# Optimization experiments

Measured on AMD Instinct MI355X. Metric: run time of the kernel, lower is better.

Reference implementation:

```python
import jax, jax.numpy as jnp
import numpy as np
import math

B, NG, LS, E = 2, 8, 512, 1024
NH = 16
HD = E // NH
EPS = 1e-6


def rms_norm(x, w):
    xf = x.astype(jnp.float32)
    n = xf * jax.lax.rsqrt(jnp.mean(xf * xf, axis=-1, keepdims=True) + EPS)
    return n.astype(x.dtype) * w


def rotate(x):
    # pairs (a,b) -> (-b, a), matching view(...,-1,2).flip(-1); x[...,0]*=-1
    x2 = x.reshape(*x.shape[:-1], HD // 2, 2)
    out = jnp.stack([-x2[..., 1], x2[..., 0]], axis=-1)
    return out.reshape(x.shape)


def setup_inputs() -> dict:
    key = jax.random.key(0)
    k1, k2, k3 = jax.random.split(key, 3)
    x = jax.random.normal(k1, (B, NG, LS, E), dtype=jnp.float32)
    W_qkv = jax.random.normal(k2, (E, 3 * E), dtype=jnp.float32) * (1.0 / math.sqrt(E))
    ln_w = jnp.ones((E,), dtype=jnp.float32)
    W_proj = jax.random.normal(k3, (E, E), dtype=jnp.float32) * (1.0 / math.sqrt(E))
    return {"x": x, "W_qkv": W_qkv, "ln_w": ln_w, "W_proj": W_proj}


def reference(x, W_qkv, ln_w, W_proj):
    b, ng, ls, _ = x.shape
    qkv = jnp.einsum('bgsc,ce->bgse', x, W_qkv)  # fused QKV projection
    q, k, v = jnp.split(qkv, 3, axis=-1)
    # QK RMSNorm over full embedding dim (before head split)
    q = rms_norm(q, ln_w)
    k = rms_norm(k, ln_w)
    # [B, ng, nh, ls, hd]
    q = q.reshape(b, ng, ls, NH, HD).swapaxes(2, 3)
    k = k.reshape(b, ng, ls, NH, HD).swapaxes(2, 3)
    v = v.reshape(b, ng, ls, NH, HD).swapaxes(2, 3)
    # RoPE (repo's variant: angles duplicated across halves, adjacent-pair rotate)
    pos = 10000.0 ** ((-2.0 * jnp.arange(0, HD, 2, dtype=jnp.float32) - 1.0) / HD)
    token_seq = jnp.arange(ls, dtype=jnp.float32)[:, None] * pos[None, :]  # [ls, hd/2]
    rot = jnp.concatenate([token_seq, token_seq], axis=-1)  # [ls, hd]
    cos, sin = jnp.cos(rot), jnp.sin(rot)
    q = q * cos + rotate(q) * sin
    k = k * cos + rotate(k) * sin
    # causal attention, scale = 1/sqrt(head_dim) (muP=False)
    scale = 1.0 / math.sqrt(HD)
    scores = jnp.einsum('bgnqd,bgnkd->bgnqk', q, k) * scale
    causal = jnp.tril(jnp.ones((ls, ls), dtype=bool))
    scores = jnp.where(causal, scores, jnp.finfo(scores.dtype).min)
    att = jax.nn.softmax(scores, axis=-1)
    y = jnp.einsum('bgnqk,bgnkd->bgnqd', att, v)
    y = y.swapaxes(2, 3).reshape(b, ng, ls, E)
    y = jnp.einsum('bgse,ef->bgsf', y, W_proj)
    return y
```

## Files before the change

kernel.cpp:

```cpp
#include <hip/hip_runtime.h>

typedef unsigned short u16;
typedef unsigned int   u32;
typedef __attribute__((ext_vector_type(8))) short bf16x8;
typedef __attribute__((ext_vector_type(4))) float f32x4;

#define MFMA16(a,b,c) __builtin_amdgcn_mfma_f32_16x16x32_bf16((a),(b),(c),0,0,0)
#define GLD16(gp, lp) __builtin_amdgcn_global_load_lds((const __attribute__((address_space(1))) u32*)(gp), (__attribute__((address_space(3))) u32*)(lp), 16, 0, 0)

#define B_   2
#define NG_  8
#define LS_  512
#define E_   1024
#define NH_  16
#define HD_  64
#define NTOK 8192

__device__ __forceinline__ u16 f2bu(float f){
  u32 u = __builtin_bit_cast(u32, f);
  u32 r = u + 0x7FFFu + ((u >> 16) & 1u);
  return (u16)(r >> 16);
}
__device__ __forceinline__ float b2f(u16 h){
  u32 u = ((u32)h) << 16;
  return __builtin_bit_cast(float, u);
}
__device__ __forceinline__ u32 pk2(float lo, float hi){
  u32 r; asm("v_cvt_pk_bf16_f32 %0, %1, %2" : "=v"(r) : "v"(lo), "v"(hi)); return r;
}

__global__ __launch_bounds__(256) void k_conv_x(const float* __restrict__ x, u16* __restrict__ xb){
  int i = blockIdx.x * 256 + threadIdx.x;
  float4 v = ((const float4*)x)[i];
  ((ushort4*)xb)[i] = make_ushort4(f2bu(v.x), f2bu(v.y), f2bu(v.z), f2bu(v.w));
}

__global__ __launch_bounds__(256) void k_transpose(const float* __restrict__ W, u16* __restrict__ WT,
                                                   int Kd, int Nd){
  __shared__ float tile[32][33];
  int tx = threadIdx.x & 31, ty = threadIdx.x >> 5;
  int c0 = blockIdx.x * 32, r0 = blockIdx.y * 32;
  #pragma unroll
  for (int i = 0; i < 4; i++)
    tile[ty + i*8][tx] = W[(size_t)(r0 + ty + i*8) * Nd + c0 + tx];
  __syncthreads();
  #pragma unroll
  for (int i = 0; i < 4; i++)
    WT[(size_t)(c0 + ty + i*8) * Kd + r0 + tx] = f2bu(tile[tx][ty + i*8]);
}

__global__ __launch_bounds__(256) void k_rope_table(float* __restrict__ ct, float* __restrict__ st){
  int i = blockIdx.x * 256 + threadIdx.x;
  int s = i >> 6, d = i & 63, j = d & 31;
  float freq = powf(10000.f, -(4.f * (float)j + 1.f) / 64.f);
  float th = (float)s * freq;
  ct[i] = cosf(th);
  st[i] = sinf(th);
}

template <typename OutT>
__global__ __launch_bounds__(256, 2) void k_gemm_bt(const u16* __restrict__ A, const u16* __restrict__ Bt,
                                                    OutT* __restrict__ C, int M, int N, int K){
  int nbn = N >> 7;
  int cpx = gridDim.x >> 3;
  int bid = (blockIdx.x & 7) * cpx + (blockIdx.x >> 3);
  int tm = bid / nbn, tn = bid % nbn;
  int tid = threadIdx.x;
  int w = tid >> 6, l = tid & 63;
  int lr = l & 15, lg = l >> 4;
  int wm = (w >> 1) * 64, wn = (w & 1) * 64;

  __shared__ u16 smem[2][2][128 * 64];

  const u16* Ab = A  + (size_t)(tm * 128) * K;
  const u16* Bb = Bt + (size_t)(tn * 128) * K;
  int NT = K >> 6;

  int srow0 = tid >> 3, ssl = tid & 7;
  auto stage = [&](int t, int s){
    int k0 = t << 6;
    #pragma unroll
    for (int q = 0; q < 4; q++){
      int row = q * 32 + srow0;
      int sc  = (ssl ^ (row & 7)) << 3;
      GLD16(Ab + (size_t)row * K + k0 + sc, &smem[s][0][q * 2048 + tid * 8]);
    }
    #pragma unroll
    for (int q = 0; q < 4; q++){
      int row = q * 32 + srow0;
      int sc  = (ssl ^ (row & 7)) << 3;
      GLD16(Bb + (size_t)row * K + k0 + sc, &smem[s][1][q * 2048 + tid * 8]);
    }
  };

  f32x4 acc[4][4] = {};

  stage(0, 0);
  stage(1, 1);
  asm volatile("s_waitcnt vmcnt(8)" ::: "memory");
  asm volatile("s_barrier" ::: "memory");

  for (int t = 0; t < NT; t++){
    int s = t & 1;
    const u16* As = smem[s][0];
    const u16* Bs = smem[s][1];
    bf16x8 bfr[4][2], afr[2][2];
    #pragma unroll
    for (int j = 0; j < 4; j++){
      int rb = wn + j * 16 + lr;
      #pragma unroll
      for (int kk = 0; kk < 2; kk++)
        bfr[j][kk] = *(const bf16x8*)&Bs[rb * 64 + ((kk * 32 + lg * 8) ^ ((rb & 7) << 3))];
    }
    #pragma unroll
    for (int i = 0; i < 2; i++){
      int ra = wm + i * 16 + lr;
      #pragma unroll
      for (int kk = 0; kk < 2; kk++)
        afr[i][kk] = *(const bf16x8*)&As[ra * 64 + ((kk * 32 + lg * 8) ^ ((ra & 7) << 3))];
    }
    __builtin_amdgcn_s_setprio(1);
    #pragma unroll
    for (int i = 0; i < 2; i++)
      #pragma unroll
      for (int j = 0; j < 4; j++){
        acc[i][j] = MFMA16(afr[i][0], bfr[j][0], acc[i][j]);
        acc[i][j] = MFMA16(afr[i][1], bfr[j][1], acc[i][j]);
      }
    __builtin_amdgcn_s_setprio(0);
    asm volatile("s_barrier" ::: "memory");
    #pragma unroll
    for (int i = 0; i < 2; i++){
      int ra = wm + (i + 2) * 16 + lr;
      #pragma unroll
      for (int kk = 0; kk < 2; kk++)
        afr[i][kk] = *(const bf16x8*)&As[ra * 64 + ((kk * 32 + lg * 8) ^ ((ra & 7) << 3))];
    }
    __builtin_amdgcn_s_setprio(1);
    #pragma unroll
    for (int i = 0; i < 2; i++)
      #pragma unroll
      for (int j = 0; j < 4; j++){
        acc[i + 2][j] = MFMA16(afr[i][0], bfr[j][0], acc[i + 2][j]);
        acc[i + 2][j] = MFMA16(afr[i][1], bfr[j][1], acc[i + 2][j]);
      }
    __builtin_amdgcn_s_setprio(0);
    asm volatile("s_barrier" ::: "memory");
    if (t + 2 < NT){
      stage(t + 2, s);
      asm volatile("s_waitcnt vmcnt(8)" ::: "memory");
      asm volatile("s_barrier" ::: "memory");
    } else if (t + 2 == NT){
      asm volatile("s_waitcnt vmcnt(0)" ::: "memory");
      asm volatile("s_barrier" ::: "memory");
    }
  }

  #pragma unroll
  for (int i = 0; i < 4; i++)
    #pragma unroll
    for (int j = 0; j < 4; j++)
      #pragma unroll
      for (int r = 0; r < 4; r++){
        int row = tm * 128 + wm + i * 16 + lg * 4 + r;
        int col = tn * 128 + wn + j * 16 + lr;
        float v = acc[i][j][r];
        if constexpr (sizeof(OutT) == 2) C[(size_t)row * N + col] = f2bu(v);
        else                             C[(size_t)row * N + col] = v;
      }
}

__global__ __launch_bounds__(256) void k_norm_rope(const u16* __restrict__ qkv, const float* __restrict__ lnw,
                                                   const float* __restrict__ ct, const float* __restrict__ st,
                                                   u16* __restrict__ qh, u16* __restrict__ kh, u16* __restrict__ vh){
  int tok = blockIdx.x;
  int t = threadIdx.x;
  int s = tok & (LS_ - 1);
  int bg = tok >> 9;
  const u16* row = qkv + (size_t)tok * 3072;
  int e0 = t * 4;

  ushort4 q4 = *(const ushort4*)&row[e0];
  ushort4 k4 = *(const ushort4*)&row[1024 + e0];
  ushort4 v4 = *(const ushort4*)&row[2048 + e0];
  float qf[4] = {b2f(q4.x), b2f(q4.y), b2f(q4.z), b2f(q4.w)};
  float kf[4] = {b2f(k4.x), b2f(k4.y), b2f(k4.z), b2f(k4.w)};

  float qss = 0.f, kss = 0.f;
  #pragma unroll
  for (int j = 0; j < 4; j++){ qss += qf[j]*qf[j]; kss += kf[j]*kf[j]; }
  #pragma unroll
  for (int o = 32; o; o >>= 1){ qss += __shfl_down(qss, o); kss += __shfl_down(kss, o); }
  __shared__ float redq[4], redk[4];
  if ((t & 63) == 0){ redq[t >> 6] = qss; redk[t >> 6] = kss; }
  __syncthreads();
  float qsum = redq[0] + redq[1] + redq[2] + redq[3];
  float ksum = redk[0] + redk[1] + redk[2] + redk[3];
  float qr = rsqrtf(qsum * (1.f / 1024.f) + 1e-6f);
  float kr = rsqrtf(ksum * (1.f / 1024.f) + 1e-6f);

  float qn[4], kn[4];
  #pragma unroll
  for (int j = 0; j < 4; j++){
    float wv = lnw[e0 + j];
    qn[j] = qf[j] * qr * wv;
    kn[j] = kf[j] * kr * wv;
  }
  int d0 = e0 & 63, h = e0 >> 6;
  const float* cr = ct + s * 64 + d0;
  const float* sr = st + s * 64 + d0;
  float qo[4], ko[4];
  #pragma unroll
  for (int p = 0; p < 4; p += 2){
    float c0 = cr[p], s0 = sr[p], c1 = cr[p+1], s1 = sr[p+1];
    qo[p]   = qn[p]   * c0 - qn[p+1] * s0;
    qo[p+1] = qn[p+1] * c1 + qn[p]   * s1;
    ko[p]   = kn[p]   * c0 - kn[p+1] * s0;
    ko[p+1] = kn[p+1] * c1 + kn[p]   * s1;
  }
  size_t oidx = (((size_t)bg * NH_ + h) * LS_ + s) * HD_ + d0;
  *(ushort4*)&qh[oidx] = make_ushort4(f2bu(qo[0]*0.125f), f2bu(qo[1]*0.125f), f2bu(qo[2]*0.125f), f2bu(qo[3]*0.125f));
  *(ushort4*)&kh[oidx] = make_ushort4(f2bu(ko[0]), f2bu(ko[1]), f2bu(ko[2]), f2bu(ko[3]));
  *(ushort4*)&vh[oidx] = v4;
}

__global__ __launch_bounds__(256) void k_vt(const u16* __restrict__ vh, u16* __restrict__ vt){
  int head = blockIdx.x >> 3, sb = blockIdx.x & 7;
  int s0 = sb * 64;
  __shared__ u16 t[64 * 72];
  const u16* src = vh + (size_t)head * LS_ * HD_ + (size_t)s0 * HD_;
  u16* dst = vt + (size_t)head * HD_ * LS_;
  #pragma unroll
  for (int p = 0; p < 2; p++){
    int idx = p * 256 + threadIdx.x;
    int r = idx >> 3, c8 = (idx & 7) * 8;
    *(bf16x8*)&t[r * 72 + c8] = *(const bf16x8*)&src[r * HD_ + c8];
  }
  __syncthreads();
  #pragma unroll
  for (int p = 0; p < 2; p++){
    int idx = p * 256 + threadIdx.x;
    int d = idx >> 3, s8 = (idx & 7) * 8;
    u16 tmp[8];
    #pragma unroll
    for (int j = 0; j < 8; j++) tmp[j] = t[(s8 + j) * 72 + d];
    *(bf16x8*)&dst[(size_t)d * LS_ + s0 + s8] = *(bf16x8*)tmp;
  }
}

__global__ __launch_bounds__(64) void k_attn(const u16* __restrict__ qh, const u16* __restrict__ kh,
                                             const u16* __restrict__ vt, u16* __restrict__ ytok){
  int bid = blockIdx.x;
  int head = bid & 255;
  int j = 15 - (bid >> 8);
  int l = threadIdx.x & 63;
  int lr = l & 15, lg = l >> 4;
  int q0 = j * 32;
  int ntw = (j >> 1) + 1;

  const u16* Qp = qh + (size_t)head * LS_ * HD_;
  const u16* Kp = kh + (size_t)head * LS_ * HD_;
  const u16* Vp = vt + (size_t)head * HD_ * LS_;
  int bg = head >> 4, h = head & 15;
  u16* Yb = ytok + (size_t)bg * LS_ * E_ + h * HD_;

  bf16x8 aq[2][2];
  #pragma unroll
  for (int mi = 0; mi < 2; mi++)
    #pragma unroll
    for (int kk = 0; kk < 2; kk++)
      aq[mi][kk] = *(const bf16x8*)&Qp[(q0 + mi*16 + lr) * 64 + kk * 32 + lg * 8];

  __shared__ u16 Pw[32 * 72];

  f32x4 o[2][4] = {};
  float mrun[2] = {-1e30f, -1e30f}, lrun[2] = {0.f, 0.f};

  bf16x8 kr[4][2];
  auto loadK = [&](int kv0){
    #pragma unroll
    for (int nk = 0; nk < 4; nk++){
      kr[nk][0] = *(const bf16x8*)&Kp[(kv0 + nk*16 + lr) * 64 + lg * 8];
      kr[nk][1] = *(const bf16x8*)&Kp[(kv0 + nk*16 + lr) * 64 + 32 + lg * 8];
    }
  };
  loadK(0);

  for (int tkv = 0; tkv < ntw; tkv++){
    int kv0 = tkv * 64;
    f32x4 sa[2][4] = {};
    __builtin_amdgcn_s_setprio(1);
    #pragma unroll
    for (int nk = 0; nk < 4; nk++)
      #pragma unroll
      for (int mi = 0; mi < 2; mi++){
        sa[mi][nk] = MFMA16(kr[nk][0], aq[mi][0], sa[mi][nk]);
        sa[mi][nk] = MFMA16(kr[nk][1], aq[mi][1], sa[mi][nk]);
      }
    __builtin_amdgcn_s_setprio(0);
    if (tkv + 1 < ntw) loadK(kv0 + 64);
    bf16x8 vr[4][2];
    #pragma unroll
    for (int nd = 0; nd < 4; nd++){
      vr[nd][0] = *(const bf16x8*)&Vp[(nd*16 + lr) * 512 + kv0 + lg * 8];
      vr[nd][1] = *(const bf16x8*)&Vp[(nd*16 + lr) * 512 + kv0 + 32 + lg * 8];
    }
    if (kv0 + 63 > q0){
      #pragma unroll
      for (int mi = 0; mi < 2; mi++){
        int qg = q0 + mi*16 + lr;
        #pragma unroll
        for (int nk = 0; nk < 4; nk++)
          #pragma unroll
          for (int r = 0; r < 4; r++){
            int kg = kv0 + nk*16 + lg*4 + r;
            if (kg > qg) sa[mi][nk][r] = -1e30f;
          }
      }
    }
    float pmax[2];
    #pragma unroll
    for (int mi = 0; mi < 2; mi++){
      float pm = sa[mi][0][0];
      #pragma unroll
      for (int nk = 0; nk < 4; nk++)
        #pragma unroll
        for (int r = 0; r < 4; r++) pm = fmaxf(pm, sa[mi][nk][r]);
      pm = fmaxf(pm, __shfl_xor(pm, 16));
      pm = fmaxf(pm, __shfl_xor(pm, 32));
      pmax[mi] = pm;
    }
    float dm = fmaxf(pmax[0] - mrun[0], pmax[1] - mrun[1]);
    if (!__all(dm <= 8.f)){
      float alpha[2];
      #pragma unroll
      for (int mi = 0; mi < 2; mi++){
        float mnew = fmaxf(mrun[mi], pmax[mi]);
        alpha[mi] = __expf(mrun[mi] - mnew);
        mrun[mi] = mnew;
        lrun[mi] *= alpha[mi];
      }
      #pragma unroll
      for (int r = 0; r < 4; r++){
        float a0 = __shfl(alpha[0], lg * 4 + r);
        float a1 = __shfl(alpha[1], lg * 4 + r);
        #pragma unroll
        for (int nd = 0; nd < 4; nd++){ o[0][nd][r] *= a0; o[1][nd][r] *= a1; }
      }
    }
    #pragma unroll
    for (int mi = 0; mi < 2; mi++){
      float psum = 0.f;
      #pragma unroll
      for (int nk = 0; nk < 4; nk++)
        #pragma unroll
        for (int r = 0; r < 4; r++){
          float pv = __expf(sa[mi][nk][r] - mrun[mi]);
          sa[mi][nk][r] = pv;
          psum += pv;
        }
      psum += __shfl_xor(psum, 16);
      psum += __shfl_xor(psum, 32);
      lrun[mi] += psum;
    }
    #pragma unroll
    for (int mi = 0; mi < 2; mi++)
      #pragma unroll
      for (int nk = 0; nk < 4; nk++){
        *(u32*)&Pw[(mi*16 + lr) * 72 + nk * 16 + lg * 4]     = pk2(sa[mi][nk][0], sa[mi][nk][1]);
        *(u32*)&Pw[(mi*16 + lr) * 72 + nk * 16 + lg * 4 + 2] = pk2(sa[mi][nk][2], sa[mi][nk][3]);
      }
    bf16x8 pa[2][2];
    #pragma unroll
    for (int mi = 0; mi < 2; mi++){
      pa[mi][0] = *(const bf16x8*)&Pw[(mi*16 + lr) * 72 + lg * 8];
      pa[mi][1] = *(const bf16x8*)&Pw[(mi*16 + lr) * 72 + 32 + lg * 8];
    }
    __builtin_amdgcn_s_setprio(1);
    #pragma unroll
    for (int nd = 0; nd < 4; nd++)
      #pragma unroll
      for (int mi = 0; mi < 2; mi++){
        o[mi][nd] = MFMA16(pa[mi][0], vr[nd][0], o[mi][nd]);
        o[mi][nd] = MFMA16(pa[mi][1], vr[nd][1], o[mi][nd]);
      }
    __builtin_amdgcn_s_setprio(0);
  }

  #pragma unroll
  for (int mi = 0; mi < 2; mi++){
    float linv = 1.f / lrun[mi];
    #pragma unroll
    for (int r = 0; r < 4; r++){
      float ir = __shfl(linv, lg * 4 + r);
      int qg = q0 + mi*16 + lg * 4 + r;
      #pragma unroll
      for (int nd = 0; nd < 4; nd++)
        Yb[(size_t)qg * E_ + nd * 16 + lr] = f2bu(o[mi][nd][r] * ir);
    }
  }
}

extern "C" void kernel_launch(void* const* d_in, const int* in_sizes, int n_in,
                              void* d_out, int out_size, void* d_ws, size_t ws_size,
                              hipStream_t stream){
  const float* x     = (const float*)d_in[0];
  const float* Wqkv  = (const float*)d_in[1];
  const float* lnw   = (const float*)d_in[2];
  const float* Wproj = (const float*)d_in[3];
  float* out = (float*)d_out;

  u16* p = (u16*)d_ws;
  u16* xb     = p; p += (size_t)NTOK * E_;
  u16* wqkvT  = p; p += (size_t)3 * E_ * E_;
  u16* wprojT = p; p += (size_t)E_ * E_;
  u16* qkv    = p; p += (size_t)NTOK * 3 * E_;
  u16* qhp    = p; p += (size_t)NTOK * E_;
  u16* khp    = p; p += (size_t)NTOK * E_;
  u16* vhp    = p; p += (size_t)NTOK * E_;
  float* ct = (float*)p;
  float* st = ct + LS_ * HD_;
  u16* vtp = qkv;

  k_conv_x<<<8192, 256, 0, stream>>>(x, xb);
  k_transpose<<<dim3(96, 32), 256, 0, stream>>>(Wqkv, wqkvT, 1024, 3072);
  k_transpose<<<dim3(32, 32), 256, 0, stream>>>(Wproj, wprojT, 1024, 1024);
  k_rope_table<<<128, 256, 0, stream>>>(ct, st);
  k_gemm_bt<u16><<<64 * 24, 256, 0, stream>>>(xb, wqkvT, qkv, NTOK, 3 * E_, E_);
  k_norm_rope<<<NTOK, 256, 0, stream>>>(qkv, lnw, ct, st, qhp, khp, vhp);
  k_vt<<<2048, 256, 0, stream>>>(vhp, vtp);
  k_attn<<<4096, 64, 0, stream>>>(qhp, khp, vtp, xb);
  k_gemm_bt<float><<<64 * 8, 256, 0, stream>>>(xb, wprojT, out, NTOK, E_, E_);
}
```

Baseline: 166.6 us.

## Enlarge GEMM tiles to 128x256 with 8 waves and triple-buffered B

Replaces the 128x128, 4-wave GEMM with a 128x256, 8-wave kernel. The B tile is triple-buffered and the A tile double-buffered, with their loads issued at different points in the loop and vmcnt waits adjusted to match. The intent is more operand reuse per block and fewer global loads per FLOP, giving better overlap of loads with MFMA work. In exchange each block uses more LDS (about 128KB), the grid holds fewer blocks (768 and 256), and the hand-tuned waitcnt counts carry a risk of races.

```diff
diff --git a/kernel.cpp b/kernel.cpp
--- a/kernel.cpp
+++ b/kernel.cpp
@@ -59,112 +59,112 @@
 }
 
 template <typename OutT>
-__global__ __launch_bounds__(256, 2) void k_gemm_bt(const u16* __restrict__ A, const u16* __restrict__ Bt,
-                                                    OutT* __restrict__ C, int M, int N, int K){
-  int nbn = N >> 7;
+__global__ __launch_bounds__(512, 2) void k_gemm_big(const u16* __restrict__ A, const u16* __restrict__ Bt,
+                                                     OutT* __restrict__ C, int M, int N, int K){
+  int nbn = N >> 8;
   int cpx = gridDim.x >> 3;
   int bid = (blockIdx.x & 7) * cpx + (blockIdx.x >> 3);
   int tm = bid / nbn, tn = bid % nbn;
   int tid = threadIdx.x;
   int w = tid >> 6, l = tid & 63;
   int lr = l & 15, lg = l >> 4;
-  int wm = (w >> 1) * 64, wn = (w & 1) * 64;
-
-  __shared__ u16 smem[2][2][128 * 64];
+  int wr = w >> 2, wc = w & 3;
+
+  __shared__ u16 sA[2][128 * 64];
+  __shared__ u16 sB[3][256 * 64];
 
   const u16* Ab = A  + (size_t)(tm * 128) * K;
-  const u16* Bb = Bt + (size_t)(tn * 128) * K;
+  const u16* Bb = Bt + (size_t)(tn * 256) * K;
   int NT = K >> 6;
 
-  int srow0 = tid >> 3, ssl = tid & 7;
-  auto stage = [&](int t, int s){
+  int rowt = tid >> 3, slot = tid & 7;
+  auto stageA = [&](int t, int b){
     int k0 = t << 6;
     #pragma unroll
+    for (int q = 0; q < 2; q++){
+      int row = q * 64 + rowt;
+      int sc = (slot ^ (row & 7)) << 3;
+      GLD16(Ab + (size_t)row * K + k0 + sc, &sA[b][q * 4096 + tid * 8]);
+    }
+  };
+  auto stageB = [&](int t, int b){
+    int k0 = t << 6;
+    #pragma unroll
     for (int q = 0; q < 4; q++){
-      int row = q * 32 + srow0;
-      int sc  = (ssl ^ (row & 7)) << 3;
-      GLD16(Ab + (size_t)row * K + k0 + sc, &smem[s][0][q * 2048 + tid * 8]);
-    }
-    #pragma unroll
-    for (int q = 0; q < 4; q++){
-      int row = q * 32 + srow0;
-      int sc  = (ssl ^ (row & 7)) << 3;
-      GLD16(Bb + (size_t)row * K + k0 + sc, &smem[s][1][q * 2048 + tid * 8]);
+      int row = q * 64 + rowt;
+      int sc = (slot ^ (row & 7)) << 3;
+      GLD16(Bb + (size_t)row * K + k0 + sc, &sB[b][q * 4096 + tid * 8]);
     }
   };
 
   f32x4 acc[4][4] = {};
 
-  stage(0, 0);
-  stage(1, 1);
-  asm volatile("s_waitcnt vmcnt(8)" ::: "memory");
-  asm volatile("s_barrier" ::: "memory");
+  stageB(0, 0); stageA(0, 0);
+  stageB(1, 1); stageA(1, 1);
 
   for (int t = 0; t < NT; t++){
-    int s = t & 1;
-    const u16* As = smem[s][0];
-    const u16* Bs = smem[s][1];
-    bf16x8 bfr[4][2], afr[2][2];
-    #pragma unroll
-    for (int j = 0; j < 4; j++){
-      int rb = wn + j * 16 + lr;
+    if (t + 2 < NT) stageB(t + 2, (t + 2) % 3);
+    if (t + 2 < NT)       asm volatile("s_waitcnt vmcnt(10)" ::: "memory");
+    else if (t + 2 == NT) asm volatile("s_waitcnt vmcnt(6)"  ::: "memory");
+    else                  asm volatile("s_waitcnt vmcnt(0)"  ::: "memory");
+    asm volatile("s_barrier" ::: "memory");
+
+    const u16* As = sA[t & 1];
+    const u16* Bs = sB[t % 3];
+    bf16x8 afr[4][2], bfr[2][2];
+    #pragma unroll
+    for (int m = 0; m < 4; m++){
+      int ra = wr * 64 + m * 16 + lr;
       #pragma unroll
       for (int kk = 0; kk < 2; kk++)
-        bfr[j][kk] = *(const bf16x8*)&Bs[rb * 64 + ((kk * 32 + lg * 8) ^ ((rb & 7) << 3))];
-    }
-    #pragma unroll
-    for (int i = 0; i < 2; i++){
-      int ra = wm + i * 16 + lr;
+        afr[m][kk] = *(const bf16x8*)&As[ra * 64 + ((kk * 32 + lg * 8) ^ ((ra & 7) << 3))];
+    }
+    #pragma unroll
+    for (int n = 0; n < 2; n++){
+      int rb = wc * 64 + n * 16 + lr;
       #pragma unroll
       for (int kk = 0; kk < 2; kk++)
-        afr[i][kk] = *(const bf16x8*)&As[ra * 64 + ((kk * 32 + lg * 8) ^ ((ra & 7) << 3))];
+        bfr[n][kk] = *(const bf16x8*)&Bs[rb * 64 + ((kk * 32 + lg * 8) ^ ((rb & 7) << 3))];
     }
     __builtin_amdgcn_s_setprio(1);
     #pragma unroll
-    for (int i = 0; i < 2; i++)
-      #pragma unroll
-      for (int j = 0; j < 4; j++){
-        acc[i][j] = MFMA16(afr[i][0], bfr[j][0], acc[i][j]);
-        acc[i][j] = MFMA16(afr[i][1], bfr[j][1], acc[i][j]);
+    for (int m = 0; m < 4; m++)
+      #pragma unroll
+      for (int n = 0; n < 2; n++){
+        acc[m][n] = MFMA16(afr[m][0], bfr[n][0], acc[m][n]);
+        acc[m][n] = MFMA16(afr[m][1], bfr[n][1], acc[m][n]);
       }
     __builtin_amdgcn_s_setprio(0);
     asm volatile("s_barrier" ::: "memory");
-    #pragma unroll
-    for (int i = 0; i < 2; i++){
-      int ra = wm + (i + 2) * 16 + lr;
+    if (t + 2 < NT) stageA(t + 2, t & 1);
+    #pragma unroll
+    for (int n = 0; n < 2; n++){
+      int rb = wc * 64 + (n + 2) * 16 + lr;
       #pragma unroll
       for (int kk = 0; kk < 2; kk++)
-        afr[i][kk] = *(const bf16x8*)&As[ra * 64 + ((kk * 32 + lg * 8) ^ ((ra & 7) << 3))];
+        bfr[n][kk] = *(const bf16x8*)&Bs[rb * 64 + ((kk * 32 + lg * 8) ^ ((rb & 7) << 3))];
     }
     __builtin_amdgcn_s_setprio(1);
     #pragma unroll
-    for (int i = 0; i < 2; i++)
-      #pragma unroll
-      for (int j = 0; j < 4; j++){
-        acc[i + 2][j] = MFMA16(afr[i][0], bfr[j][0], acc[i + 2][j]);
-        acc[i + 2][j] = MFMA16(afr[i][1], bfr[j][1], acc[i + 2][j]);
+    for (int m = 0; m < 4; m++)
+      #pragma unroll
+      for (int n = 0; n < 2; n++){
+        acc[m][n + 2] = MFMA16(afr[m][0], bfr[n][0], acc[m][n + 2]);
+        acc[m][n + 2] = MFMA16(afr[m][1], bfr[n][1], acc[m][n + 2]);
       }
     __builtin_amdgcn_s_setprio(0);
     asm volatile("s_barrier" ::: "memory");
-    if (t + 2 < NT){
-      stage(t + 2, s);
-      asm volatile("s_waitcnt vmcnt(8)" ::: "memory");
-      asm volatile("s_barrier" ::: "memory");
-    } else if (t + 2 == NT){
-      asm volatile("s_waitcnt vmcnt(0)" ::: "memory");
-      asm volatile("s_barrier" ::: "memory");
-    }
-  }
-
-  #pragma unroll
-  for (int i = 0; i < 4; i++)
-    #pragma unroll
-    for (int j = 0; j < 4; j++)
+  }
+
+  #pragma unroll
+  for (int m = 0; m < 4; m++)
+    #pragma unroll
+    for (int n = 0; n < 4; n++)
       #pragma unroll
       for (int r = 0; r < 4; r++){
-        int row = tm * 128 + wm + i * 16 + lg * 4 + r;
-        int col = tn * 128 + wn + j * 16 + lr;
-        float v = acc[i][j][r];
+        int row = tm * 128 + wr * 64 + m * 16 + lg * 4 + r;
+        int col = tn * 256 + wc * 64 + n * 16 + lr;
+        float v = acc[m][n][r];
         if constexpr (sizeof(OutT) == 2) C[(size_t)row * N + col] = f2bu(v);
         else                             C[(size_t)row * N + col] = v;
       }
@@ -426,9 +426,9 @@
   k_transpose<<<dim3(96, 32), 256, 0, stream>>>(Wqkv, wqkvT, 1024, 3072);
   k_transpose<<<dim3(32, 32), 256, 0, stream>>>(Wproj, wprojT, 1024, 1024);
   k_rope_table<<<128, 256, 0, stream>>>(ct, st);
-  k_gemm_bt<u16><<<64 * 24, 256, 0, stream>>>(xb, wqkvT, qkv, NTOK, 3 * E_, E_);
+  k_gemm_big<u16><<<768, 512, 0, stream>>>(xb, wqkvT, qkv, NTOK, 3 * E_, E_);
   k_norm_rope<<<NTOK, 256, 0, stream>>>(qkv, lnw, ct, st, qhp, khp, vhp);
   k_vt<<<2048, 256, 0, stream>>>(vhp, vtp);
   k_attn<<<4096, 64, 0, stream>>>(qhp, khp, vtp, xb);
-  k_gemm_bt<float><<<64 * 8, 256, 0, stream>>>(xb, wprojT, out, NTOK, E_, E_);
-}
+  k_gemm_big<float><<<256, 512, 0, stream>>>(xb, wprojT, out, NTOK, E_, E_);
+}
```

After: 202.8 us. 21.8% more time.
